# Kernel optimization log

Measured on AMD Instinct MI355X. Metric: run time of the kernel, lower is better.

## Reference

```python
import jax, jax.numpy as jnp
import numpy as np

D = 128  # hard-coded hidden dim in MLP_T

def setup_inputs() -> dict:
    key = jax.random.key(0)
    ks = jax.random.split(key, 8)
    N, IN = 16384, 768
    return {
        "x": jax.random.normal(ks[0], (N, IN), dtype=jnp.float32),
        "decay_value": 1,
        "W_token": jax.random.normal(ks[1], (IN, D), dtype=jnp.float32) * (IN ** -0.5),
        "b_token": jax.random.normal(ks[2], (D,), dtype=jnp.float32) * 0.02,
        "W_qkv": jax.random.normal(ks[3], (D, 3 * D), dtype=jnp.float32) * (D ** -0.5),
        "b_qkv": jax.random.normal(ks[4], (3 * D,), dtype=jnp.float32) * 0.02,
        "W_fc": jax.random.normal(ks[5], (D, 1), dtype=jnp.float32) * (D ** -0.5),
        "b_fc": jax.random.normal(ks[6], (1,), dtype=jnp.float32) * 0.02,
    }

def reference(x, decay_value, W_token, b_token, W_qkv, b_qkv, W_fc, b_fc):
    # token projection: [N, in_chan] -> [N, 128]
    h = x @ W_token + b_token
    # qkv: [N, 384] split along feature dim into q, k, v of [N, 128]
    qkv = h @ W_qkv + b_qkv
    q, k, v = qkv[:, :D], qkv[:, D:2 * D], qkv[:, 2 * D:]
    # sigmoid attention (no row normalization); dropout is identity in eval mode
    att_scores = jax.nn.sigmoid(q @ k.T)            # [N, N]
    att = att_scores @ v                            # [N, 128]
    out = att @ W_fc + b_fc                         # [N, 1]
    # GradientReversal is identity in the forward pass
    return out
```

## Files before the change

### kernel.cpp

```cpp
#include <hip/hip_runtime.h>
#include <hip/hip_bf16.h>
#include <stdint.h>

#define N_ROWS 16384

typedef __bf16 bf16x8 __attribute__((ext_vector_type(8)));
typedef float f32x4 __attribute__((ext_vector_type(4)));

#define AS1 __attribute__((address_space(1)))
#define AS3 __attribute__((address_space(3)))

#define OFF_WCS  0u
#define OFF_BC   589824u
#define OFF_QB   591360u
#define OFF_KB   4785664u
#define OFF_WV   8979968u
#define OFF_PART 9045504u

__global__ void prep(const float* __restrict__ Wt, const float* __restrict__ Wq,
                     const float* __restrict__ bt, const float* __restrict__ bq,
                     __bf16* __restrict__ WcS, float* __restrict__ bc) {
    int u = blockIdx.x * 256 + threadIdx.x;
    if (u < 768 * 96) {
        int k = u / 96, n4 = u % 96;
        float s[4] = {0, 0, 0, 0};
        const float* wtp = Wt + k * 128;
        const float* wqp = Wq + n4 * 4;
#pragma unroll 8
        for (int d = 0; d < 128; d++) {
            float a = wtp[d];
            float4 b = *(const float4*)(wqp + d * 384);
            s[0] += a * b.x; s[1] += a * b.y; s[2] += a * b.z; s[3] += a * b.w;
        }
        int kb_ = k >> 6, c = (k >> 3) & 7, k7 = k & 7;
#pragma unroll
        for (int j = 0; j < 4; j++) {
            int n = n4 * 4 + j;
            WcS[n * 768 + kb_ * 64 + ((c ^ (n & 7)) << 3) + k7] = (__bf16)s[j];
        }
    }
    if (u < 384) {
        float s = bq[u];
        for (int d = 0; d < 128; d++) s += bt[d] * Wq[d * 384 + u];
        bc[u] = s;
    }
}

__launch_bounds__(256)
__global__ void gemm_qkv(const float* __restrict__ x, const __bf16* __restrict__ WcS,
                         const float* __restrict__ bc, const float* __restrict__ W_fc,
                         __bf16* __restrict__ qb, __bf16* __restrict__ kb,
                         float* __restrict__ wv) {
    __shared__ float  Asm[64 * 64];
    __shared__ __bf16 Bsm[128 * 64];
    __shared__ float  wred[64];
    const int tid = threadIdx.x, wave = tid >> 6, lane = tid & 63;
    const int n16 = lane & 15, q = lane >> 4;
    const int mh = wave >> 1, nw = wave & 1;
    const int row0 = blockIdx.x * 64;
    const int sp = blockIdx.y;

    const char* aptr[4];
    const char* bptr[4];
    {
        int p = (lane & 15) >> 1, half = lane & 1;
#pragma unroll
        for (int i = 0; i < 4; i++) {
            int ar = row0 + wave * 16 + i * 4 + (lane >> 4);
            aptr[i] = (const char*)x + (size_t)ar * 3072 + ((p ^ (ar & 7)) * 8 + half * 4) * 4;
            int br = sp * 128 + wave * 32 + i * 8 + (lane >> 3);
            bptr[i] = (const char*)WcS + (size_t)br * 1536 + (lane & 7) * 16;
        }
    }
    f32x4 acc[2][4];
#pragma unroll
    for (int mt = 0; mt < 2; mt++)
#pragma unroll
        for (int t = 0; t < 4; t++) acc[mt][t] = (f32x4){0, 0, 0, 0};

    for (int kbi = 0; kbi < 12; kbi++) {
#pragma unroll
        for (int i = 0; i < 4; i++)
            __builtin_amdgcn_global_load_lds((const AS1 void*)(aptr[i] + kbi * 256),
                (AS3 void*)((char*)Asm + wave * 4096 + i * 1024), 16, 0, 0);
#pragma unroll
        for (int i = 0; i < 4; i++)
            __builtin_amdgcn_global_load_lds((const AS1 void*)(bptr[i] + kbi * 128),
                (AS3 void*)((char*)Bsm + wave * 4096 + i * 1024), 16, 0, 0);
        __syncthreads();
#pragma unroll
        for (int ks = 0; ks < 2; ks++) {
            const int swz = ((ks * 4 + q) ^ (n16 & 7)) << 3;
            bf16x8 af[2];
#pragma unroll
            for (int mt = 0; mt < 2; mt++) {
                const float* ap = Asm + (mh * 32 + mt * 16 + n16) * 64 + swz;
                f32x4 a0 = *(const f32x4*)ap;
                f32x4 a1 = *(const f32x4*)(ap + 4);
                bf16x8 t;
                t[0] = (__bf16)a0[0]; t[1] = (__bf16)a0[1]; t[2] = (__bf16)a0[2]; t[3] = (__bf16)a0[3];
                t[4] = (__bf16)a1[0]; t[5] = (__bf16)a1[1]; t[6] = (__bf16)a1[2]; t[7] = (__bf16)a1[3];
                af[mt] = t;
            }
#pragma unroll
            for (int t = 0; t < 4; t++) {
                bf16x8 bf = *(const bf16x8*)(Bsm + (nw * 64 + t * 16 + n16) * 64 + swz);
                acc[0][t] = __builtin_amdgcn_mfma_f32_16x16x32_bf16(af[0], bf, acc[0][t], 0, 0, 0);
                acc[1][t] = __builtin_amdgcn_mfma_f32_16x16x32_bf16(af[1], bf, acc[1][t], 0, 0, 0);
            }
        }
        __syncthreads();
    }

    const int clb = nw * 64 + n16;
    if (sp == 0) {
#pragma unroll
        for (int t = 0; t < 4; t++) {
            int cl = clb + t * 16;
            float bcv = bc[cl];
#pragma unroll
            for (int mt = 0; mt < 2; mt++)
#pragma unroll
                for (int r = 0; r < 4; r++) {
                    int row = row0 + mh * 32 + mt * 16 + q * 4 + r;
                    qb[row * 128 + cl] = (__bf16)((acc[mt][t][r] + bcv) * -1.44269504088896f);
                }
        }
    } else if (sp == 1) {
#pragma unroll
        for (int t = 0; t < 4; t++) {
            int d = clb + t * 16;
            float bcv = bc[128 + d];
#pragma unroll
            for (int mt = 0; mt < 2; mt++)
#pragma unroll
                for (int r = 0; r < 4; r++) {
                    int row = row0 + mh * 32 + mt * 16 + q * 4 + r;
                    kb[row * 128 + (((d >> 3) ^ (row & 15)) << 3) + (d & 7)] = (__bf16)(acc[mt][t][r] + bcv);
                }
        }
    } else {
        float wacc[2][4] = {{0, 0, 0, 0}, {0, 0, 0, 0}};
#pragma unroll
        for (int t = 0; t < 4; t++) {
            int cl = clb + t * 16;
            float bcv = bc[256 + cl];
            float wf = W_fc[cl];
#pragma unroll
            for (int mt = 0; mt < 2; mt++)
#pragma unroll
                for (int r = 0; r < 4; r++) wacc[mt][r] += (acc[mt][t][r] + bcv) * wf;
        }
        float vred[2][4];
#pragma unroll
        for (int mt = 0; mt < 2; mt++)
#pragma unroll
            for (int r = 0; r < 4; r++) {
                float v = wacc[mt][r];
                v += __shfl_xor(v, 1, 64);
                v += __shfl_xor(v, 2, 64);
                v += __shfl_xor(v, 4, 64);
                v += __shfl_xor(v, 8, 64);
                vred[mt][r] = v;
                if (nw == 0 && n16 == 0) wred[mh * 32 + mt * 16 + q * 4 + r] = v;
            }
        __syncthreads();
        if (nw == 1 && n16 == 0) {
#pragma unroll
            for (int mt = 0; mt < 2; mt++)
#pragma unroll
                for (int r = 0; r < 4; r++) {
                    int lr = mh * 32 + mt * 16 + q * 4 + r;
                    wv[row0 + lr] = wred[lr] + vred[mt][r];
                }
        }
    }
}

__launch_bounds__(128, 4)
__global__ void attn(const __bf16* __restrict__ qb, const __bf16* __restrict__ kb,
                     const float* __restrict__ wv, float* __restrict__ partial) {
    __shared__ __bf16 kbuf[2 * 32 * 128];
    __shared__ float wbuf[2 * 32];
    const int tid = threadIdx.x;
    const int wave = tid >> 6, lane = tid & 63;
    const int n16 = lane & 15, q = lane >> 4;
    const int row0 = blockIdx.x * 64 + wave * 32;
    const int sp = blockIdx.y;
    const int jb0 = sp * 2048;

    bf16x8 qf[2][4];
#pragma unroll
    for (int mt = 0; mt < 2; mt++)
#pragma unroll
        for (int ks = 0; ks < 4; ks++)
            qf[mt][ks] = *(const bf16x8*)(qb + (row0 + mt * 16 + n16) * 128 + ks * 32 + q * 8);
    float acc[2][4] = {{0}, {0}};

    {
        const char* gsrc = (const char*)kb + (size_t)jb0 * 256;
        float w0 = wv[jb0 + (tid & 31)];
#pragma unroll
        for (int i = 0; i < 4; i++) {
            const int off = wave * 4096 + i * 1024;
            __builtin_amdgcn_global_load_lds((const AS1 void*)(gsrc + off + lane * 16),
                                             (AS3 void*)((char*)kbuf + off), 16, 0, 0);
        }
        if (tid < 32) wbuf[tid] = w0;
        __syncthreads();
    }

#pragma unroll 2
    for (int jc = 0; jc < 64; jc++) {
        const int cb = jc & 1;
        const __bf16* curK = kbuf + cb * (32 * 128);
        __bf16* nxtK = kbuf + (cb ^ 1) * (32 * 128);
        const float* curW = wbuf + cb * 32;
        float* nxtW = wbuf + (cb ^ 1) * 32;
        const int jn = (jc + 1 < 64) ? jc + 1 : 63;

        float wnext = wv[jb0 + jn * 32 + (tid & 31)];
        const char* gsrc = (const char*)kb + (size_t)(jb0 + jn * 32) * 256;
#pragma unroll
        for (int i = 0; i < 4; i++) {
            const int off = wave * 4096 + i * 1024;
            __builtin_amdgcn_global_load_lds((const AS1 void*)(gsrc + off + lane * 16),
                                             (AS3 void*)((char*)nxtK + off), 16, 0, 0);
        }

#pragma unroll
        for (int t = 0; t < 2; t++) {
            f32x4 s0 = (f32x4){0, 0, 0, 0}, s1 = (f32x4){0, 0, 0, 0};
#pragma unroll
            for (int ks = 0; ks < 4; ks++) {
                const int chunk = (ks * 4 + q) ^ n16;
                bf16x8 bf = *(const bf16x8*)(curK + (t * 16 + n16) * 128 + chunk * 8);
                s0 = __builtin_amdgcn_mfma_f32_16x16x32_bf16(qf[0][ks], bf, s0, 0, 0, 0);
                s1 = __builtin_amdgcn_mfma_f32_16x16x32_bf16(qf[1][ks], bf, s1, 0, 0, 0);
            }
            const float wval = curW[t * 16 + n16];
#pragma unroll
            for (int r = 0; r < 4; r++) {
                acc[0][r] += __builtin_amdgcn_rcpf(1.0f + __builtin_amdgcn_exp2f(s0[r])) * wval;
                acc[1][r] += __builtin_amdgcn_rcpf(1.0f + __builtin_amdgcn_exp2f(s1[r])) * wval;
            }
        }

        if (tid < 32) nxtW[tid] = wnext;
        __syncthreads();
    }

#pragma unroll
    for (int mt = 0; mt < 2; mt++)
#pragma unroll
        for (int r = 0; r < 4; r++) {
            float v = acc[mt][r];
            v += __shfl_xor(v, 1, 64);
            v += __shfl_xor(v, 2, 64);
            v += __shfl_xor(v, 4, 64);
            v += __shfl_xor(v, 8, 64);
            if (n16 == 0) partial[sp * N_ROWS + row0 + mt * 16 + q * 4 + r] = v;
        }
}

__global__ void reduce_out(const float* __restrict__ partial, const float* __restrict__ b_fc,
                           float* __restrict__ out) {
    int i = blockIdx.x * 256 + threadIdx.x;
    float v = b_fc[0];
#pragma unroll
    for (int s = 0; s < 8; s++) v += partial[s * N_ROWS + i];
    out[i] = v;
}

extern "C" void kernel_launch(void* const* d_in, const int* in_sizes, int n_in,
                              void* d_out, int out_size, void* d_ws, size_t ws_size,
                              hipStream_t stream) {
    const float* x       = (const float*)d_in[0];
    const float* W_token = (const float*)d_in[2];
    const float* b_token = (const float*)d_in[3];
    const float* W_qkv   = (const float*)d_in[4];
    const float* b_qkv   = (const float*)d_in[5];
    const float* W_fc    = (const float*)d_in[6];
    const float* b_fc    = (const float*)d_in[7];
    float* out = (float*)d_out;
    char* ws = (char*)d_ws;

    __bf16* WcS = (__bf16*)(ws + OFF_WCS);
    float*  bc  = (float*)(ws + OFF_BC);
    __bf16* qb  = (__bf16*)(ws + OFF_QB);
    __bf16* kb  = (__bf16*)(ws + OFF_KB);
    float*  wv  = (float*)(ws + OFF_WV);
    float*  part = (float*)(ws + OFF_PART);

    prep<<<288, 256, 0, stream>>>(W_token, W_qkv, b_token, b_qkv, WcS, bc);
    gemm_qkv<<<dim3(256, 3), 256, 0, stream>>>(x, WcS, bc, W_fc, qb, kb, wv);
    attn<<<dim3(256, 8), 128, 0, stream>>>(qb, kb, wv, part);
    reduce_out<<<64, 256, 0, stream>>>(part, b_fc, out);
}
```

Before: 218.9 us.

## Deepen attention K pipeline to 4-slot ring with 256-thread blocks

The attention kernel now uses 4 waves per block (128 query rows), so each K tile staged in LDS serves twice as many rows. Staging is a 4-slot LDS ring that prefetches two chunks ahead. Each iteration uses one explicit vmcnt wait plus one barrier, replacing the double buffer that needed a sync after compute. The weight vector wv is read directly from global memory instead of being staged in LDS. The grid is flattened with the split index in the low bits, so neighbouring blocks share query rows. This is meant to hide K load latency and cut barrier cost, at the price of more LDS per block and extra global loads of wv each iteration.

```diff
diff --git a/kernel.cpp b/kernel.cpp
--- a/kernel.cpp
+++ b/kernel.cpp
@@ -177,16 +177,17 @@
     }
 }
 
-__launch_bounds__(128, 4)
+__launch_bounds__(256, 4)
 __global__ void attn(const __bf16* __restrict__ qb, const __bf16* __restrict__ kb,
                      const float* __restrict__ wv, float* __restrict__ partial) {
-    __shared__ __bf16 kbuf[2 * 32 * 128];
-    __shared__ float wbuf[2 * 32];
+    __shared__ __bf16 kbuf[4 * 32 * 128];
     const int tid = threadIdx.x;
     const int wave = tid >> 6, lane = tid & 63;
     const int n16 = lane & 15, q = lane >> 4;
-    const int row0 = blockIdx.x * 64 + wave * 32;
-    const int sp = blockIdx.y;
+    const int bid = blockIdx.x;
+    const int sp = bid & 7;
+    const int rb = bid >> 3;
+    const int row0 = rb * 128 + wave * 32;
     const int jb0 = sp * 2048;
 
     bf16x8 qf[2][4];
@@ -194,40 +195,32 @@
     for (int mt = 0; mt < 2; mt++)
 #pragma unroll
         for (int ks = 0; ks < 4; ks++)
-            qf[mt][ks] = *(const bf16x8*)(qb + (row0 + mt * 16 + n16) * 128 + ks * 32 + q * 8);
+            qf[mt][ks] = *(const bf16x8*)(qb + (size_t)(row0 + mt * 16 + n16) * 128 + ks * 32 + q * 8);
+
     float acc[2][4] = {{0}, {0}};
 
-    {
-        const char* gsrc = (const char*)kb + (size_t)jb0 * 256;
-        float w0 = wv[jb0 + (tid & 31)];
-#pragma unroll
-        for (int i = 0; i < 4; i++) {
-            const int off = wave * 4096 + i * 1024;
-            __builtin_amdgcn_global_load_lds((const AS1 void*)(gsrc + off + lane * 16),
-                                             (AS3 void*)((char*)kbuf + off), 16, 0, 0);
-        }
-        if (tid < 32) wbuf[tid] = w0;
-        __syncthreads();
-    }
-
-#pragma unroll 2
+#define ISSUE(c, slot)                                                                  \
+    {                                                                                   \
+        const char* gsrc = (const char*)kb + (size_t)(jb0 + (c) * 32) * 256 + wave * 2048; \
+        char* gdst = (char*)kbuf + (slot) * 8192 + wave * 2048;                          \
+        __builtin_amdgcn_global_load_lds((const AS1 void*)(gsrc + lane * 16),            \
+                                         (AS3 void*)gdst, 16, 0, 0);                     \
+        __builtin_amdgcn_global_load_lds((const AS1 void*)(gsrc + 1024 + lane * 16),     \
+                                         (AS3 void*)(gdst + 1024), 16, 0, 0);            \
+    }
+
+    ISSUE(0, 0);
+    ISSUE(1, 1);
+
     for (int jc = 0; jc < 64; jc++) {
-        const int cb = jc & 1;
-        const __bf16* curK = kbuf + cb * (32 * 128);
-        __bf16* nxtK = kbuf + (cb ^ 1) * (32 * 128);
-        const float* curW = wbuf + cb * 32;
-        float* nxtW = wbuf + (cb ^ 1) * 32;
-        const int jn = (jc + 1 < 64) ? jc + 1 : 63;
-
-        float wnext = wv[jb0 + jn * 32 + (tid & 31)];
-        const char* gsrc = (const char*)kb + (size_t)(jb0 + jn * 32) * 256;
-#pragma unroll
-        for (int i = 0; i < 4; i++) {
-            const int off = wave * 4096 + i * 1024;
-            __builtin_amdgcn_global_load_lds((const AS1 void*)(gsrc + off + lane * 16),
-                                             (AS3 void*)((char*)nxtK + off), 16, 0, 0);
-        }
-
+        const int jn = (jc + 2 < 64) ? jc + 2 : 63;
+        ISSUE(jn, (jc + 2) & 3);
+
+        asm volatile("s_waitcnt vmcnt(4)" ::: "memory");
+        __builtin_amdgcn_sched_barrier(0);
+        __builtin_amdgcn_s_barrier();
+
+        const __bf16* curK = kbuf + (jc & 3) * 4096;
 #pragma unroll
         for (int t = 0; t < 2; t++) {
             f32x4 s0 = (f32x4){0, 0, 0, 0}, s1 = (f32x4){0, 0, 0, 0};
@@ -238,17 +231,15 @@
                 s0 = __builtin_amdgcn_mfma_f32_16x16x32_bf16(qf[0][ks], bf, s0, 0, 0, 0);
                 s1 = __builtin_amdgcn_mfma_f32_16x16x32_bf16(qf[1][ks], bf, s1, 0, 0, 0);
             }
-            const float wval = curW[t * 16 + n16];
+            const float wval = wv[jb0 + jc * 32 + t * 16 + n16];
 #pragma unroll
             for (int r = 0; r < 4; r++) {
                 acc[0][r] += __builtin_amdgcn_rcpf(1.0f + __builtin_amdgcn_exp2f(s0[r])) * wval;
                 acc[1][r] += __builtin_amdgcn_rcpf(1.0f + __builtin_amdgcn_exp2f(s1[r])) * wval;
             }
         }
-
-        if (tid < 32) nxtW[tid] = wnext;
-        __syncthreads();
-    }
+    }
+#undef ISSUE
 
 #pragma unroll
     for (int mt = 0; mt < 2; mt++)
@@ -294,6 +285,6 @@
 
     prep<<<288, 256, 0, stream>>>(W_token, W_qkv, b_token, b_qkv, WcS, bc);
     gemm_qkv<<<dim3(256, 3), 256, 0, stream>>>(x, WcS, bc, W_fc, qb, kb, wv);
-    attn<<<dim3(256, 8), 128, 0, stream>>>(qb, kb, wv, part);
+    attn<<<1024, 256, 0, stream>>>(qb, kb, wv, part);
     reduce_out<<<64, 256, 0, stream>>>(part, b_fc, out);
 }
```

Result: faster. 203.8 us (-6.9%).
